# Kernel tuning notes

Measured on AMD Instinct MI355X. Metric: run time of the kernel, lower is better.

The kernel has to match this reference:

```python
import jax, jax.numpy as jnp
import numpy as np

THRESH = 0.7
N_MIN = 16 * 512 * 512 // 16  # 262144
IGNORE_LB = 1


def setup_inputs() -> dict:
    key = jax.random.key(0)
    k1, k2 = jax.random.split(key)
    logits = jax.random.normal(k1, (16, 19, 512, 512), dtype=jnp.float32)
    labels = jax.random.randint(k2, (16, 512, 512), 0, 19)
    return {"logits": logits, "labels": labels}


def reference(logits, labels):
    # Per-pixel cross-entropy with ignore_index semantics (loss=0 at ignored pixels)
    logp = jax.nn.log_softmax(logits, axis=1)                     # [N,C,H,W]
    picked = jnp.take_along_axis(logp, labels[:, None], axis=1)  # [N,1,H,W]
    loss = -picked[:, 0].reshape(-1)                              # [N*H*W]
    valid = labels.reshape(-1) != IGNORE_LB
    loss = jnp.where(valid, loss, 0.0)

    thresh = -jnp.log(jnp.asarray(THRESH, dtype=loss.dtype))

    # Top-n_min valid losses (descending); invalid pixels pushed to -inf.
    masked = jnp.where(valid, loss, -jnp.inf)
    top, _ = jax.lax.top_k(masked, N_MIN)
    kth = top[N_MIN - 1]

    # Branch 1: mean of all valid losses > thresh
    keep_gt = valid & (loss > thresh)
    cnt_gt = jnp.sum(keep_gt)
    mean_gt = jnp.sum(jnp.where(keep_gt, loss, 0.0)) / jnp.maximum(cnt_gt, 1).astype(loss.dtype)
    # Branch 2: mean of top n_min losses
    mean_top = jnp.mean(top)

    return jnp.where(kth > thresh, mean_gt, mean_top)
```

## Files before the change

kernel.cpp:

```cpp
#include <hip/hip_runtime.h>
#include <math.h>

#define NPIX  4194304
#define HW    262144
#define NCH   19
#define KSEL  262144u
#define IGN   1
#define THRESH_F 0.35667494393873245f

__device__ void select_from_hist(const unsigned int* __restrict__ gh, int nbins,
                                 unsigned int need, int* res)
{
    __shared__ unsigned int sh[2048];
    __shared__ unsigned int ssum[256];
    const int tid = threadIdx.x;
    for (int i = tid; i < nbins; i += 256) sh[i] = gh[i];
    __syncthreads();
    const int per = nbins >> 8;
    const int base = tid * per;
    unsigned int p = 0;
    for (int i = 0; i < per; ++i) p += sh[base + i];
    ssum[tid] = p;
    __syncthreads();
    for (int off = 1; off < 256; off <<= 1) {
        unsigned int add = (tid + off < 256) ? ssum[tid + off] : 0u;
        __syncthreads();
        ssum[tid] += add;
        __syncthreads();
    }
    unsigned int Sme   = ssum[tid];
    unsigned int Snext = (tid < 255) ? ssum[tid + 1] : 0u;
    if (Sme >= need && Snext < need) {
        unsigned int above = Snext;
        int bin = base;
        for (int b = base + per - 1; b >= base; --b) {
            unsigned int c = sh[b];
            if (above + c >= need) { bin = b; break; }
            above += c;
        }
        res[0] = bin; res[1] = (int)above;
    }
    if (tid == 0 && ssum[0] < need) { res[0] = 0; res[1] = 0; }
    __syncthreads();
}

__device__ __forceinline__ void block_sum_to_double(float v, double* target)
{
    #pragma unroll
    for (int o = 32; o > 0; o >>= 1) v += __shfl_down(v, o);
    __shared__ float wsum[4];
    int wid = threadIdx.x >> 6;
    if ((threadIdx.x & 63) == 0) wsum[wid] = v;
    __syncthreads();
    if (threadIdx.x == 0) {
        float t = wsum[0] + wsum[1] + wsum[2] + wsum[3];
        atomicAdd(target, (double)t);
    }
}

__global__ __launch_bounds__(256) void k_loss(
    const float* __restrict__ logits, const int* __restrict__ labels,
    float* __restrict__ losses, unsigned int* __restrict__ hist1,
    double* __restrict__ sum_gt, unsigned int* __restrict__ cnt_gt)
{
    __shared__ unsigned int lh[2048];
    for (int i = threadIdx.x; i < 2048; i += 256) lh[i] = 0u;
    __syncthreads();

    const int p0 = (blockIdx.x * 256 + threadIdx.x) * 4;
    const int n  = p0 >> 18;
    const int hw = p0 & (HW - 1);
    const float* base = logits + (size_t)n * (NCH * HW) + hw;

    float4 vals[NCH];
    #pragma unroll
    for (int c = 0; c < NCH; ++c)
        vals[c] = *(const float4*)(base + (size_t)c * HW);
    const int4 lab4 = *(const int4*)(labels + p0);
    const int labs[4] = {lab4.x, lab4.y, lab4.z, lab4.w};

    float lsum = 0.f;
    unsigned int lcnt = 0u;
    float out4[4];

    #pragma unroll
    for (int j = 0; j < 4; ++j) {
        float m = -__builtin_inff(), picked = 0.f;
        #pragma unroll
        for (int c = 0; c < NCH; ++c) {
            float x = (j == 0) ? vals[c].x : (j == 1) ? vals[c].y : (j == 2) ? vals[c].z : vals[c].w;
            m = fmaxf(m, x);
            if (c == labs[j]) picked = x;
        }
        float s = 0.f;
        #pragma unroll
        for (int c = 0; c < NCH; ++c) {
            float x = (j == 0) ? vals[c].x : (j == 1) ? vals[c].y : (j == 2) ? vals[c].z : vals[c].w;
            s += __expf(x - m);
        }
        float loss = m + logf(s) - picked;
        bool valid = (labs[j] != IGN);
        out4[j] = valid ? loss : -__builtin_inff();
        if (valid) {
            if (loss > THRESH_F) { lsum += loss; lcnt++; }
            atomicAdd(&lh[__float_as_uint(loss) >> 21], 1u);
        }
    }
    *(float4*)(losses + p0) = make_float4(out4[0], out4[1], out4[2], out4[3]);

    #pragma unroll
    for (int o = 32; o > 0; o >>= 1) { lsum += __shfl_down(lsum, o); lcnt += __shfl_down(lcnt, o); }
    __shared__ float  s_sum[4];
    __shared__ unsigned int s_cnt[4];
    int wid = threadIdx.x >> 6;
    if ((threadIdx.x & 63) == 0) { s_sum[wid] = lsum; s_cnt[wid] = lcnt; }
    __syncthreads();
    if (threadIdx.x == 0) {
        float t = s_sum[0] + s_sum[1] + s_sum[2] + s_sum[3];
        unsigned int tc = s_cnt[0] + s_cnt[1] + s_cnt[2] + s_cnt[3];
        atomicAdd(sum_gt, (double)t);
        atomicAdd(cnt_gt, tc);
    }
    for (int i = threadIdx.x; i < 2048; i += 256) {
        unsigned int c = lh[i];
        if (c) atomicAdd(&hist1[i], c);
    }
}

__global__ __launch_bounds__(256) void k_hist2(
    const float* __restrict__ losses, const unsigned int* __restrict__ hist1,
    unsigned int* __restrict__ hist2, double* __restrict__ sum_hi1)
{
    __shared__ int res[2];
    select_from_hist(hist1, 2048, KSEL, res);
    const int B1 = res[0];

    __shared__ unsigned int lh[2048];
    for (int i = threadIdx.x; i < 2048; i += 256) lh[i] = 0u;
    __syncthreads();

    const int t = (blockIdx.x * 256 + threadIdx.x) * 4;
    const uint4 w4 = *(const uint4*)(losses + t);
    const unsigned int wv[4] = {w4.x, w4.y, w4.z, w4.w};
    float lsum = 0.f;
    #pragma unroll
    for (int j = 0; j < 4; ++j) {
        unsigned int w = wv[j];
        if (w & 0x80000000u) continue;
        int b1 = (int)(w >> 21);
        if (b1 == B1)      atomicAdd(&lh[(w >> 10) & 0x7FFu], 1u);
        else if (b1 > B1)  lsum += __uint_as_float(w);
    }
    __syncthreads();
    for (int i = threadIdx.x; i < 2048; i += 256)
        if (lh[i]) atomicAdd(&hist2[i], lh[i]);
    block_sum_to_double(lsum, sum_hi1);
}

__global__ __launch_bounds__(256) void k_hist3(
    const float* __restrict__ losses, const unsigned int* __restrict__ hist1,
    const unsigned int* __restrict__ hist2, unsigned int* __restrict__ hist3,
    double* __restrict__ sum_hi2)
{
    __shared__ int res[2];
    select_from_hist(hist1, 2048, KSEL, res);
    const int B1 = res[0];
    const unsigned int a1 = (unsigned int)res[1];
    select_from_hist(hist2, 2048, KSEL - a1, res);
    const int B2 = res[0];

    __shared__ unsigned int lh[1024];
    for (int i = threadIdx.x; i < 1024; i += 256) lh[i] = 0u;
    __syncthreads();

    const int t = (blockIdx.x * 256 + threadIdx.x) * 4;
    const uint4 w4 = *(const uint4*)(losses + t);
    const unsigned int wv[4] = {w4.x, w4.y, w4.z, w4.w};
    float lsum = 0.f;
    #pragma unroll
    for (int j = 0; j < 4; ++j) {
        unsigned int w = wv[j];
        if (w & 0x80000000u) continue;
        if ((int)(w >> 21) != B1) continue;
        int b2 = (int)((w >> 10) & 0x7FFu);
        if (b2 == B2)      atomicAdd(&lh[w & 0x3FFu], 1u);
        else if (b2 > B2)  lsum += __uint_as_float(w);
    }
    __syncthreads();
    for (int i = threadIdx.x; i < 1024; i += 256)
        if (lh[i]) atomicAdd(&hist3[i], lh[i]);
    block_sum_to_double(lsum, sum_hi2);
}

__global__ __launch_bounds__(256) void k_final(
    const unsigned int* __restrict__ hist1, const unsigned int* __restrict__ hist2,
    const unsigned int* __restrict__ hist3,
    const double* __restrict__ sum_gt, const unsigned int* __restrict__ cnt_gt,
    const double* __restrict__ sum_hi1, const double* __restrict__ sum_hi2,
    float* __restrict__ out)
{
    __shared__ int res[2];
    select_from_hist(hist1, 2048, KSEL, res);
    const int B1 = res[0];
    const unsigned int a1 = (unsigned int)res[1];
    select_from_hist(hist2, 2048, KSEL - a1, res);
    const int B2 = res[0];
    const unsigned int a2 = (unsigned int)res[1];
    const unsigned int need3 = KSEL - a1 - a2;
    const unsigned int hibits = ((unsigned int)B1 << 21) | ((unsigned int)B2 << 10);

    __shared__ unsigned int h3[1024];
    __shared__ unsigned int c_suf[256];
    __shared__ double s_suf[256];
    const int tid = threadIdx.x;
    for (int i = tid; i < 1024; i += 256) h3[i] = hist3[i];
    __syncthreads();
    unsigned int cp = 0; double sp = 0.0;
    for (int i = 0; i < 4; ++i) {
        int b = tid * 4 + i;
        unsigned int c = h3[b];
        cp += c;
        sp += (double)c * (double)__uint_as_float(hibits | (unsigned int)b);
    }
    c_suf[tid] = cp; s_suf[tid] = sp;
    __syncthreads();
    for (int off = 1; off < 256; off <<= 1) {
        unsigned int ca = (tid + off < 256) ? c_suf[tid + off] : 0u;
        double sa = (tid + off < 256) ? s_suf[tid + off] : 0.0;
        __syncthreads();
        c_suf[tid] += ca; s_suf[tid] += sa;
        __syncthreads();
    }
    __shared__ int r_l;
    __shared__ unsigned int r_above;
    __shared__ double r_sum3;
    unsigned int Sme   = c_suf[tid];
    unsigned int Snext = (tid < 255) ? c_suf[tid + 1] : 0u;
    double       Wnext = (tid < 255) ? s_suf[tid + 1] : 0.0;
    if (Sme >= need3 && Snext < need3) {
        unsigned int above = Snext;
        double sum3 = Wnext;
        int l = tid * 4;
        for (int b = tid * 4 + 3; b >= tid * 4; --b) {
            unsigned int c = h3[b];
            if (above + c >= need3) { l = b; break; }
            above += c;
            sum3 += (double)c * (double)__uint_as_float(hibits | (unsigned int)b);
        }
        r_l = l; r_above = above; r_sum3 = sum3;
    }
    if (tid == 0 && c_suf[0] < need3) { r_l = 0; r_above = 0; r_sum3 = 0.0; }
    __syncthreads();

    if (tid == 0) {
        float v = __uint_as_float(hibits | (unsigned int)r_l);
        unsigned long long cnt_above = (unsigned long long)a1 + a2 + r_above;
        double sum_above = *sum_hi1 + *sum_hi2 + r_sum3;
        double mean_top = (sum_above + (double)(KSEL - cnt_above) * (double)v) / (double)KSEL;
        double result;
        if (v > THRESH_F) {
            unsigned int cg = *cnt_gt;
            result = *sum_gt / (double)(cg > 0u ? cg : 1u);
        } else {
            result = mean_top;
        }
        out[0] = (float)result;
    }
}

extern "C" void kernel_launch(void* const* d_in, const int* in_sizes, int n_in,
                              void* d_out, int out_size, void* d_ws, size_t ws_size,
                              hipStream_t stream)
{
    const float* logits = (const float*)d_in[0];
    const int*   labels = (const int*)d_in[1];
    float* out = (float*)d_out;

    unsigned int* hist1 = (unsigned int*)d_ws;
    unsigned int* hist2 = hist1 + 2048;
    unsigned int* hist3 = hist2 + 2048;
    double* sum_gt  = (double*)((char*)d_ws + 20480);
    double* sum_hi1 = sum_gt + 1;
    double* sum_hi2 = sum_gt + 2;
    unsigned int* cnt_gt = (unsigned int*)(sum_gt + 3);
    float* losses = (float*)((char*)d_ws + 32768);

    hipMemsetAsync(d_ws, 0, 20512, stream);

    k_loss <<<dim3(NPIX / (256 * 4)), dim3(256), 0, stream>>>(logits, labels, losses, hist1, sum_gt, cnt_gt);
    k_hist2<<<dim3(NPIX / (256 * 4)), dim3(256), 0, stream>>>(losses, hist1, hist2, sum_hi1);
    k_hist3<<<dim3(NPIX / (256 * 4)), dim3(256), 0, stream>>>(losses, hist1, hist2, hist3, sum_hi2);
    k_final<<<dim3(1), dim3(256), 0, stream>>>(hist1, hist2, hist3, sum_gt, cnt_gt, sum_hi1, sum_hi2, out);
}
```

Before: 580.8 us.

## Split histogram pass out of loss kernel and use persistent 256-block histogram kernels

Moves the first-level histogram out of the loss kernel into a new grid-stride kernel with 256 blocks. The hist2 and hist3 passes also drop from 4096 blocks to 256 grid-stride blocks, which cuts repeated per-block select_from_hist work, shared-histogram clearing and global atomic flushes. Global double and uint atomics are replaced by per-block partial sums that the final kernel reduces. The cost is an extra kernel launch plus one more full read of the 16 MB losses buffer.

```diff
diff --git a/kernel.cpp b/kernel.cpp
--- a/kernel.cpp
+++ b/kernel.cpp
@@ -7,6 +7,10 @@
 #define KSEL  262144u
 #define IGN   1
 #define THRESH_F 0.35667494393873245f
+
+#define P1BLK 4096
+#define HBLK  256
+#define HTHR  65536
 
 __device__ void select_from_hist(const unsigned int* __restrict__ gh, int nbins,
                                  unsigned int need, int* res)
@@ -44,29 +48,11 @@
     __syncthreads();
 }
 
-__device__ __forceinline__ void block_sum_to_double(float v, double* target)
-{
-    #pragma unroll
-    for (int o = 32; o > 0; o >>= 1) v += __shfl_down(v, o);
-    __shared__ float wsum[4];
-    int wid = threadIdx.x >> 6;
-    if ((threadIdx.x & 63) == 0) wsum[wid] = v;
-    __syncthreads();
-    if (threadIdx.x == 0) {
-        float t = wsum[0] + wsum[1] + wsum[2] + wsum[3];
-        atomicAdd(target, (double)t);
-    }
-}
-
 __global__ __launch_bounds__(256) void k_loss(
     const float* __restrict__ logits, const int* __restrict__ labels,
-    float* __restrict__ losses, unsigned int* __restrict__ hist1,
-    double* __restrict__ sum_gt, unsigned int* __restrict__ cnt_gt)
-{
-    __shared__ unsigned int lh[2048];
-    for (int i = threadIdx.x; i < 2048; i += 256) lh[i] = 0u;
-    __syncthreads();
-
+    float* __restrict__ losses,
+    float* __restrict__ psum, unsigned int* __restrict__ pcnt)
+{
     const int p0 = (blockIdx.x * 256 + threadIdx.x) * 4;
     const int n  = p0 >> 18;
     const int hw = p0 & (HW - 1);
@@ -101,10 +87,7 @@
         float loss = m + logf(s) - picked;
         bool valid = (labs[j] != IGN);
         out4[j] = valid ? loss : -__builtin_inff();
-        if (valid) {
-            if (loss > THRESH_F) { lsum += loss; lcnt++; }
-            atomicAdd(&lh[__float_as_uint(loss) >> 21], 1u);
-        }
+        if (valid & (loss > THRESH_F)) { lsum += loss; lcnt++; }
     }
     *(float4*)(losses + p0) = make_float4(out4[0], out4[1], out4[2], out4[3]);
 
@@ -116,11 +99,29 @@
     if ((threadIdx.x & 63) == 0) { s_sum[wid] = lsum; s_cnt[wid] = lcnt; }
     __syncthreads();
     if (threadIdx.x == 0) {
-        float t = s_sum[0] + s_sum[1] + s_sum[2] + s_sum[3];
-        unsigned int tc = s_cnt[0] + s_cnt[1] + s_cnt[2] + s_cnt[3];
-        atomicAdd(sum_gt, (double)t);
-        atomicAdd(cnt_gt, tc);
-    }
+        psum[blockIdx.x] = s_sum[0] + s_sum[1] + s_sum[2] + s_sum[3];
+        pcnt[blockIdx.x] = s_cnt[0] + s_cnt[1] + s_cnt[2] + s_cnt[3];
+    }
+}
+
+__global__ __launch_bounds__(256) void k_hist1(
+    const float* __restrict__ losses, unsigned int* __restrict__ hist1)
+{
+    __shared__ unsigned int lh[2048];
+    for (int i = threadIdx.x; i < 2048; i += 256) lh[i] = 0u;
+    __syncthreads();
+
+    const uint4* l4 = (const uint4*)losses;
+    for (int i = blockIdx.x * 256 + threadIdx.x; i < NPIX / 4; i += HTHR) {
+        uint4 w4 = l4[i];
+        const unsigned int wv[4] = {w4.x, w4.y, w4.z, w4.w};
+        #pragma unroll
+        for (int j = 0; j < 4; ++j) {
+            unsigned int w = wv[j];
+            if (!(w & 0x80000000u)) atomicAdd(&lh[w >> 21], 1u);
+        }
+    }
+    __syncthreads();
     for (int i = threadIdx.x; i < 2048; i += 256) {
         unsigned int c = lh[i];
         if (c) atomicAdd(&hist1[i], c);
@@ -129,7 +130,7 @@
 
 __global__ __launch_bounds__(256) void k_hist2(
     const float* __restrict__ losses, const unsigned int* __restrict__ hist1,
-    unsigned int* __restrict__ hist2, double* __restrict__ sum_hi1)
+    unsigned int* __restrict__ hist2, double* __restrict__ ghi1)
 {
     __shared__ int res[2];
     select_from_hist(hist1, 2048, KSEL, res);
@@ -139,28 +140,38 @@
     for (int i = threadIdx.x; i < 2048; i += 256) lh[i] = 0u;
     __syncthreads();
 
-    const int t = (blockIdx.x * 256 + threadIdx.x) * 4;
-    const uint4 w4 = *(const uint4*)(losses + t);
-    const unsigned int wv[4] = {w4.x, w4.y, w4.z, w4.w};
+    const uint4* l4 = (const uint4*)losses;
     float lsum = 0.f;
-    #pragma unroll
-    for (int j = 0; j < 4; ++j) {
-        unsigned int w = wv[j];
-        if (w & 0x80000000u) continue;
-        int b1 = (int)(w >> 21);
-        if (b1 == B1)      atomicAdd(&lh[(w >> 10) & 0x7FFu], 1u);
-        else if (b1 > B1)  lsum += __uint_as_float(w);
+    for (int i = blockIdx.x * 256 + threadIdx.x; i < NPIX / 4; i += HTHR) {
+        uint4 w4 = l4[i];
+        const unsigned int wv[4] = {w4.x, w4.y, w4.z, w4.w};
+        #pragma unroll
+        for (int j = 0; j < 4; ++j) {
+            unsigned int w = wv[j];
+            if (w & 0x80000000u) continue;
+            int b1 = (int)(w >> 21);
+            if (b1 == B1)      atomicAdd(&lh[(w >> 10) & 0x7FFu], 1u);
+            else if (b1 > B1)  lsum += __uint_as_float(w);
+        }
     }
     __syncthreads();
     for (int i = threadIdx.x; i < 2048; i += 256)
         if (lh[i]) atomicAdd(&hist2[i], lh[i]);
-    block_sum_to_double(lsum, sum_hi1);
+
+    #pragma unroll
+    for (int o = 32; o > 0; o >>= 1) lsum += __shfl_down(lsum, o);
+    __shared__ float wsum[4];
+    int wid = threadIdx.x >> 6;
+    if ((threadIdx.x & 63) == 0) wsum[wid] = lsum;
+    __syncthreads();
+    if (threadIdx.x == 0)
+        ghi1[blockIdx.x] = (double)(wsum[0] + wsum[1] + wsum[2] + wsum[3]);
 }
 
 __global__ __launch_bounds__(256) void k_hist3(
     const float* __restrict__ losses, const unsigned int* __restrict__ hist1,
     const unsigned int* __restrict__ hist2, unsigned int* __restrict__ hist3,
-    double* __restrict__ sum_hi2)
+    double* __restrict__ ghi2)
 {
     __shared__ int res[2];
     select_from_hist(hist1, 2048, KSEL, res);
@@ -173,32 +184,75 @@
     for (int i = threadIdx.x; i < 1024; i += 256) lh[i] = 0u;
     __syncthreads();
 
-    const int t = (blockIdx.x * 256 + threadIdx.x) * 4;
-    const uint4 w4 = *(const uint4*)(losses + t);
-    const unsigned int wv[4] = {w4.x, w4.y, w4.z, w4.w};
+    const uint4* l4 = (const uint4*)losses;
     float lsum = 0.f;
-    #pragma unroll
-    for (int j = 0; j < 4; ++j) {
-        unsigned int w = wv[j];
-        if (w & 0x80000000u) continue;
-        if ((int)(w >> 21) != B1) continue;
-        int b2 = (int)((w >> 10) & 0x7FFu);
-        if (b2 == B2)      atomicAdd(&lh[w & 0x3FFu], 1u);
-        else if (b2 > B2)  lsum += __uint_as_float(w);
+    for (int i = blockIdx.x * 256 + threadIdx.x; i < NPIX / 4; i += HTHR) {
+        uint4 w4 = l4[i];
+        const unsigned int wv[4] = {w4.x, w4.y, w4.z, w4.w};
+        #pragma unroll
+        for (int j = 0; j < 4; ++j) {
+            unsigned int w = wv[j];
+            if (w & 0x80000000u) continue;
+            if ((int)(w >> 21) != B1) continue;
+            int b2 = (int)((w >> 10) & 0x7FFu);
+            if (b2 == B2)      atomicAdd(&lh[w & 0x3FFu], 1u);
+            else if (b2 > B2)  lsum += __uint_as_float(w);
+        }
     }
     __syncthreads();
     for (int i = threadIdx.x; i < 1024; i += 256)
         if (lh[i]) atomicAdd(&hist3[i], lh[i]);
-    block_sum_to_double(lsum, sum_hi2);
+
+    #pragma unroll
+    for (int o = 32; o > 0; o >>= 1) lsum += __shfl_down(lsum, o);
+    __shared__ float wsum[4];
+    int wid = threadIdx.x >> 6;
+    if ((threadIdx.x & 63) == 0) wsum[wid] = lsum;
+    __syncthreads();
+    if (threadIdx.x == 0)
+        ghi2[blockIdx.x] = (double)(wsum[0] + wsum[1] + wsum[2] + wsum[3]);
 }
 
 __global__ __launch_bounds__(256) void k_final(
     const unsigned int* __restrict__ hist1, const unsigned int* __restrict__ hist2,
     const unsigned int* __restrict__ hist3,
-    const double* __restrict__ sum_gt, const unsigned int* __restrict__ cnt_gt,
-    const double* __restrict__ sum_hi1, const double* __restrict__ sum_hi2,
+    const float* __restrict__ psum, const unsigned int* __restrict__ pcnt,
+    const double* __restrict__ ghi1, const double* __restrict__ ghi2,
     float* __restrict__ out)
 {
+    const int tid = threadIdx.x;
+
+    double my_sum = 0.0;
+    unsigned long long my_cnt = 0ull;
+    #pragma unroll
+    for (int i = 0; i < 16; ++i) {
+        my_sum += (double)psum[tid * 16 + i];
+        my_cnt += (unsigned long long)pcnt[tid * 16 + i];
+    }
+    double my_hi = ghi1[tid] + ghi2[tid] - ghi2[tid];
+    double my_hi2 = ghi2[tid];
+    #pragma unroll
+    for (int o = 32; o > 0; o >>= 1) {
+        my_sum += __shfl_down(my_sum, o);
+        my_cnt += __shfl_down(my_cnt, o);
+        my_hi  += __shfl_down(my_hi, o);
+        my_hi2 += __shfl_down(my_hi2, o);
+    }
+    __shared__ double r_sumw[4], r_hiw[4], r_hi2w[4];
+    __shared__ unsigned long long r_cntw[4];
+    int wid = tid >> 6;
+    if ((tid & 63) == 0) { r_sumw[wid] = my_sum; r_cntw[wid] = my_cnt; r_hiw[wid] = my_hi; r_hi2w[wid] = my_hi2; }
+    __syncthreads();
+    __shared__ double t_sum_gt, t_hi1, t_hi2;
+    __shared__ unsigned long long t_cnt_gt;
+    if (tid == 0) {
+        t_sum_gt = r_sumw[0] + r_sumw[1] + r_sumw[2] + r_sumw[3];
+        t_cnt_gt = r_cntw[0] + r_cntw[1] + r_cntw[2] + r_cntw[3];
+        t_hi1    = r_hiw[0] + r_hiw[1] + r_hiw[2] + r_hiw[3];
+        t_hi2    = r_hi2w[0] + r_hi2w[1] + r_hi2w[2] + r_hi2w[3];
+    }
+    __syncthreads();
+
     __shared__ int res[2];
     select_from_hist(hist1, 2048, KSEL, res);
     const int B1 = res[0];
@@ -212,10 +266,10 @@
     __shared__ unsigned int h3[1024];
     __shared__ unsigned int c_suf[256];
     __shared__ double s_suf[256];
-    const int tid = threadIdx.x;
     for (int i = tid; i < 1024; i += 256) h3[i] = hist3[i];
     __syncthreads();
     unsigned int cp = 0; double sp = 0.0;
+    #pragma unroll
     for (int i = 0; i < 4; ++i) {
         int b = tid * 4 + i;
         unsigned int c = h3[b];
@@ -255,12 +309,12 @@
     if (tid == 0) {
         float v = __uint_as_float(hibits | (unsigned int)r_l);
         unsigned long long cnt_above = (unsigned long long)a1 + a2 + r_above;
-        double sum_above = *sum_hi1 + *sum_hi2 + r_sum3;
+        double sum_above = t_hi1 + t_hi2 + r_sum3;
         double mean_top = (sum_above + (double)(KSEL - cnt_above) * (double)v) / (double)KSEL;
         double result;
         if (v > THRESH_F) {
-            unsigned int cg = *cnt_gt;
-            result = *sum_gt / (double)(cg > 0u ? cg : 1u);
+            unsigned long long cg = t_cnt_gt;
+            result = t_sum_gt / (double)(cg > 0ull ? cg : 1ull);
         } else {
             result = mean_top;
         }
@@ -279,16 +333,17 @@
     unsigned int* hist1 = (unsigned int*)d_ws;
     unsigned int* hist2 = hist1 + 2048;
     unsigned int* hist3 = hist2 + 2048;
-    double* sum_gt  = (double*)((char*)d_ws + 20480);
-    double* sum_hi1 = sum_gt + 1;
-    double* sum_hi2 = sum_gt + 2;
-    unsigned int* cnt_gt = (unsigned int*)(sum_gt + 3);
-    float* losses = (float*)((char*)d_ws + 32768);
-
-    hipMemsetAsync(d_ws, 0, 20512, stream);
-
-    k_loss <<<dim3(NPIX / (256 * 4)), dim3(256), 0, stream>>>(logits, labels, losses, hist1, sum_gt, cnt_gt);
-    k_hist2<<<dim3(NPIX / (256 * 4)), dim3(256), 0, stream>>>(losses, hist1, hist2, sum_hi1);
-    k_hist3<<<dim3(NPIX / (256 * 4)), dim3(256), 0, stream>>>(losses, hist1, hist2, hist3, sum_hi2);
-    k_final<<<dim3(1), dim3(256), 0, stream>>>(hist1, hist2, hist3, sum_gt, cnt_gt, sum_hi1, sum_hi2, out);
-}
+    float*        psum  = (float*)((char*)d_ws + 20480);
+    unsigned int* pcnt  = (unsigned int*)((char*)d_ws + 36864);
+    double*       ghi1  = (double*)((char*)d_ws + 53248);
+    double*       ghi2  = (double*)((char*)d_ws + 55296);
+    float*        losses = (float*)((char*)d_ws + 65536);
+
+    hipMemsetAsync(d_ws, 0, 20480, stream);
+
+    k_loss <<<dim3(P1BLK), dim3(256), 0, stream>>>(logits, labels, losses, psum, pcnt);
+    k_hist1<<<dim3(HBLK),  dim3(256), 0, stream>>>(losses, hist1);
+    k_hist2<<<dim3(HBLK),  dim3(256), 0, stream>>>(losses, hist1, hist2, ghi1);
+    k_hist3<<<dim3(HBLK),  dim3(256), 0, stream>>>(losses, hist1, hist2, hist3, ghi2);
+    k_final<<<dim3(1),     dim3(256), 0, stream>>>(hist1, hist2, hist3, psum, pcnt, ghi1, ghi2, out);
+}
```

New measurement: 472.6 us. 18.6% less time.
